# Kernel optimization log

Measured on AMD Instinct MI355X. Metric: run time of the kernel, lower is better.

Reference implementation:

```python
import jax, jax.numpy as jnp
import numpy as np

# Model dims (match init_kwargs)
B_, L, D_MODEL = 1, 2048, 1024
D_INNER, D_CONV, DT_RANK, D_STATE = 2048, 4, 64, 16


def setup_inputs() -> dict:
    key = jax.random.key(0)
    ks = jax.random.split(key, 8)
    s = lambda k, shape, scale: jax.random.normal(k, shape, jnp.float32) * scale
    return {
        "x": jax.random.normal(ks[0], (B_, L, D_MODEL), jnp.float32),
        "in_proj_w": s(ks[1], (D_MODEL, 2 * D_INNER), 0.02),
        "in_proj_b": jnp.zeros((2 * D_INNER,), jnp.float32),
        "conv_w": s(ks[2], (D_CONV, D_INNER), 0.1),          # depthwise kernel, one tap-vector per channel
        "conv_b": jnp.zeros((D_INNER,), jnp.float32),
        "x_proj_w": s(ks[3], (D_INNER, DT_RANK + 2 * D_STATE), 0.02),
        "dt_proj_w": s(ks[4], (DT_RANK, D_INNER), 0.1),
        "dt_proj_b": s(ks[5], (D_INNER,), 0.1),
        "A_log": jnp.log(jnp.tile(jnp.arange(1, D_STATE + 1, dtype=jnp.float32), (D_INNER, 1))),  # S4D-real init
        "D": jnp.ones((D_INNER,), jnp.float32),
        "out_proj_w": s(ks[6], (D_INNER, D_MODEL), 0.02),
        "out_proj_b": jnp.zeros((D_MODEL,), jnp.float32),
    }


def _mamba_forward(x, in_proj_w, in_proj_b, conv_w, conv_b, x_proj_w,
                   dt_proj_w, dt_proj_b, A_log, D, out_proj_w, out_proj_b):
    b, l, _ = x.shape
    d_inner = conv_w.shape[1]
    d_state = A_log.shape[1]

    # in_proj -> split into ssm path and gating residual
    x_and_res = x @ in_proj_w + in_proj_b                 # [b, l, 2*d_inner]
    xin, res = jnp.split(x_and_res, 2, axis=-1)

    # causal depthwise conv1d over the sequence dim (pad left d_conv-1, trunc to l)
    xp = jnp.pad(xin, ((0, 0), (D_CONV - 1, 0), (0, 0)))
    kern = conv_w[:, None, :]                             # [W, I=1, O=d_inner]
    xc = jax.lax.conv_general_dilated(
        xp, kern, window_strides=(1,), padding="VALID",
        dimension_numbers=("NWC", "WIO", "NWC"),
        feature_group_count=d_inner) + conv_b             # [b, l, d_inner]
    u = jax.nn.silu(xc)

    # selective SSM: input-dependent dt, B, C
    A = -jnp.exp(A_log)                                   # [d_inner, d_state]
    dbc = u @ x_proj_w                                    # [b, l, dt_rank + 2*d_state]
    dt, Bm, Cm = jnp.split(dbc, [DT_RANK, DT_RANK + d_state], axis=-1)
    delta = jax.nn.softplus(dt @ dt_proj_w + dt_proj_b)   # [b, l, d_inner]

    deltaA = jnp.exp(jnp.einsum("bld,dn->bldn", delta, A))          # [b, l, d_inner, d_state]
    deltaBu = jnp.einsum("bld,bln,bld->bldn", delta, Bm, u)         # [b, l, d_inner, d_state]

    def step(h, inp):
        dA_t, dBu_t, C_t = inp
        h = dA_t * h + dBu_t                              # [b, d_inner, d_state]
        y_t = jnp.einsum("bdn,bn->bd", h, C_t)
        return h, y_t

    h0 = jnp.zeros((b, d_inner, d_state), u.dtype)
    _, ys = jax.lax.scan(
        step, h0,
        (deltaA.transpose(1, 0, 2, 3), deltaBu.transpose(1, 0, 2, 3), Cm.transpose(1, 0, 2)))
    y = ys.transpose(1, 0, 2) + u * D                     # skip connection via D

    # gate and out-project
    y = y * jax.nn.silu(res)
    return y @ out_proj_w + out_proj_b                    # [b, l, d_model]


def reference(x, in_proj_w, in_proj_b, conv_w, conv_b, x_proj_w,
              dt_proj_w, dt_proj_b, A_log, D, out_proj_w, out_proj_b):
    return _mamba_forward(x, in_proj_w, in_proj_b, conv_w, conv_b, x_proj_w,
                          dt_proj_w, dt_proj_b, A_log, D, out_proj_w, out_proj_b)
```

## Files before the change

### kernel.cpp

```cpp
#include <hip/hip_runtime.h>


#define L_SEQ 2048
#define DMODEL 1024
#define DINNER 2048
#define NSTATE 16
#define DTRANK 64
#define NPROJ_PAD 128
#define NCH 128
#define TCH 16

typedef __attribute__((ext_vector_type(8))) short short8;
typedef __attribute__((ext_vector_type(4))) float f32x4;

__device__ __forceinline__ unsigned short f2bf(float f) {
  unsigned int u = __float_as_uint(f);
  u += 0x7FFFu + ((u >> 16) & 1u);
  return (unsigned short)(u >> 16);
}
__device__ __forceinline__ float bf2f(unsigned short u) {
  return __uint_as_float(((unsigned int)u) << 16);
}

__device__ __forceinline__ void gload16(const void* g, void* l) {
  __builtin_amdgcn_global_load_lds((const __attribute__((address_space(1))) void*)g,
                                   (__attribute__((address_space(3))) void*)l, 16, 0, 0);
}

__global__ void prep_kernel(const float* __restrict__ in_proj_w, const float* __restrict__ x_proj_w,
                            const float* __restrict__ dt_proj_w,
                            const float* __restrict__ out_proj_w, const float* __restrict__ x,
                            unsigned short* __restrict__ w1t, unsigned short* __restrict__ w3t,
                            unsigned short* __restrict__ w4t, unsigned short* __restrict__ w5t,
                            unsigned short* __restrict__ xb) {
  const int bx = blockIdx.x;
  const int tx = threadIdx.x, ty = threadIdx.y;
  const int id = ty * 32 + tx;

  if (bx >= 6464) {
    if (bx < 8512) {
      const int fid = (bx - 6464) * 256 + id;
      f32x4 v = ((const f32x4*)x)[fid];
      ushort4 o;
      o.x = f2bf(v.x); o.y = f2bf(v.y); o.z = f2bf(v.z); o.w = f2bf(v.w);
      ((ushort4*)xb)[fid] = o;
    } else {
      const int fid = (bx - 8512) * 256 + id;
      ((uint4*)(w3t + 96 * 2048))[fid] = (uint4){0, 0, 0, 0};
    }
    return;
  }

  const float* in;
  unsigned short* out;
  int R, C, rel, gx;
  if (bx < 4096) { in = in_proj_w; out = w1t; R = 1024; C = 4096; rel = bx; gx = 128; }
  else if (bx < 4288) { in = x_proj_w; out = w3t; R = 2048; C = 96; rel = bx - 4096; gx = 3; }
  else if (bx < 4416) { in = dt_proj_w; out = w4t; R = 64; C = 2048; rel = bx - 4288; gx = 64; }
  else { in = out_proj_w; out = w5t; R = 2048; C = 1024; rel = bx - 4416; gx = 32; }
  const int c0 = (rel % gx) * 32, r0 = (rel / gx) * 32;

  __shared__ float tile[32][33];
  for (int y = ty; y < 32; y += 8) tile[y][tx] = in[(size_t)(r0 + y) * C + c0 + tx];
  __syncthreads();
  for (int y = ty; y < 32; y += 8) out[(size_t)(c0 + y) * R + r0 + tx] = f2bf(tile[tx][y]);
}

__global__ void conv_silu_kernel(const unsigned short* __restrict__ xin,
                                 const float* __restrict__ cw, const float* __restrict__ cb,
                                 unsigned short* __restrict__ ub) {
  const int id = blockIdx.x * 256 + threadIdx.x;
  const int d = id & (DINNER - 1);
  const int t0 = (id >> 11) * 4;
  float xv[7];
#pragma unroll
  for (int j = 0; j < 7; j++) {
    int tt = t0 - 3 + j;
    xv[j] = (tt >= 0) ? bf2f(xin[(size_t)tt * DINNER + d]) : 0.f;
  }
  float w0 = cw[d], w1 = cw[DINNER + d], w2 = cw[2 * DINNER + d], w3 = cw[3 * DINNER + d];
  const float b = cb[d];
#pragma unroll
  for (int k = 0; k < 4; k++) {
    float acc = b + xv[k] * w0 + xv[k + 1] * w1 + xv[k + 2] * w2 + xv[k + 3] * w3;
    float s = acc / (1.f + __expf(-acc));
    ub[(size_t)(t0 + k) * DINNER + d] = f2bf(s);
  }
}

template <int EPI, int BM, int BN>
__global__ void gemm_bf16(const unsigned short* __restrict__ A,
                          const unsigned short* __restrict__ Bt, float* __restrict__ C,
                          unsigned short* __restrict__ C2, const float* __restrict__ bias, int M,
                          int N, int K, int KS) {
  constexpr int MI = BM / 32, NJ = BN / 32;
  __shared__ __align__(16) unsigned short lA[2][BM * 64];
  __shared__ __align__(16) unsigned short lB[2][BN * 64];
  const int tid = threadIdx.x;
  const int w = tid >> 6;
  const int lane = tid & 63;
  const int m0 = blockIdx.x * BM;
  const int n0 = blockIdx.y * BN;
  const int kbase = blockIdx.z * KS;
  const int lr = lane >> 3;
  const int srcoff = ((lane & 7) ^ lr) * 8;
  const int wm = (w & 1) * (BM / 2);
  const int wn = (w >> 1) * (BN / 2);
  const int ml = lane & 15;
  const int quad = lane >> 4;

  f32x4 acc[MI][NJ];
#pragma unroll
  for (int i = 0; i < MI; i++)
#pragma unroll
    for (int j = 0; j < NJ; j++) acc[i][j] = (f32x4){0.f, 0.f, 0.f, 0.f};

  const unsigned short* Ag = A + (size_t)m0 * K + kbase;
  const unsigned short* Bg = Bt + (size_t)n0 * K + kbase;

  const int niter = KS >> 6;
  auto stage = [&](int buf, int kk) {
#pragma unroll
    for (int c2 = 0; c2 < BM / 32; c2++) {
      const int row = w * (BM / 4) + c2 * 8 + lr;
      gload16(Ag + (size_t)row * K + kk + srcoff, &lA[buf][(w * (BM / 4) + c2 * 8) * 64]);
    }
#pragma unroll
    for (int c2 = 0; c2 < BN / 32; c2++) {
      const int row = w * (BN / 4) + c2 * 8 + lr;
      gload16(Bg + (size_t)row * K + kk + srcoff, &lB[buf][(w * (BN / 4) + c2 * 8) * 64]);
    }
  };

  stage(0, 0);
  for (int it = 0; it < niter; it++) {
    __syncthreads();
    if (it + 1 < niter) stage((it + 1) & 1, (it + 1) << 6);
    const unsigned short* bufA = lA[it & 1];
    const unsigned short* bufB = lB[it & 1];
#pragma unroll
    for (int ks = 0; ks < 2; ks++) {
      short8 af[MI], bfr[NJ];
#pragma unroll
      for (int i = 0; i < MI; i++) {
        const int row = wm + i * 16 + ml;
        af[i] = *(const short8*)&bufA[row * 64 + ((ks * 4 + quad) ^ (ml & 7)) * 8];
      }
#pragma unroll
      for (int j = 0; j < NJ; j++) {
        const int row = wn + j * 16 + ml;
        bfr[j] = *(const short8*)&bufB[row * 64 + ((ks * 4 + quad) ^ (ml & 7)) * 8];
      }
#pragma unroll
      for (int i = 0; i < MI; i++)
#pragma unroll
        for (int j = 0; j < NJ; j++)
          acc[i][j] = __builtin_amdgcn_mfma_f32_16x16x32_bf16(af[i], bfr[j], acc[i][j], 0, 0, 0);
    }
  }

  float* Cp = (EPI == 3) ? C + (size_t)blockIdx.z * M * N : C;
#pragma unroll
  for (int i = 0; i < MI; i++) {
#pragma unroll
    for (int j = 0; j < NJ; j++) {
      const int col = n0 + wn + j * 16 + ml;
      float bv = (EPI == 3) ? 0.f : (bias ? bias[col] : 0.f);
#pragma unroll
      for (int r = 0; r < 4; r++) {
        const int row = m0 + wm + i * 16 + quad * 4 + r;
        float v = acc[i][j][r] + bv;
        if (EPI == 0 || EPI == 3) {
          Cp[(size_t)row * N + col] = v;
        } else if (EPI == 4) {
          if (col < DINNER) {
            ((unsigned short*)C)[(size_t)row * DINNER + col] = f2bf(v);
          } else {
            float s = v / (1.f + __expf(-v));
            C2[(size_t)row * DINNER + (col - DINNER)] = f2bf(s);
          }
        } else if (EPI == 5) {
          float sp = (v > 15.f) ? v : __logf(1.f + __expf(v));
          C2[(size_t)row * N + col] = f2bf(sp);
        }
      }
    }
  }
}

__global__ void reduce_dbc_kernel(const float* __restrict__ part, float* __restrict__ dbc,
                                  unsigned short* __restrict__ dtb) {
  const int id = blockIdx.x * 256 + threadIdx.x;
  float s = 0.f;
#pragma unroll
  for (int z = 0; z < 8; z++) s += part[(size_t)z * (L_SEQ * NPROJ_PAD) + id];
  dbc[id] = s;
  const int col = id & 127;
  if (col < 64) dtb[(id >> 7) * 64 + col] = f2bf(s);
}


__device__ __forceinline__ void load_bc(const float* dbc, int c, float (&Bs)[TCH][NSTATE],
                                        float (&Cs)[TCH][NSTATE], int tid) {
  for (int idx = tid; idx < TCH * 2 * NSTATE; idx += 256) {
    int t = idx >> 5, q = idx & 31;
    float v = dbc[(size_t)(c * TCH + t) * NPROJ_PAD + DTRANK + q];
    if (q < 16) Bs[t][q] = v;
    else Cs[t][q - 16] = v;
  }
}

__global__ void scan1_kernel(const unsigned short* __restrict__ db,
                             const unsigned short* __restrict__ ub, const float* __restrict__ dbc,
                             const float* __restrict__ A_log, unsigned short* __restrict__ P,
                             unsigned short* __restrict__ Hz) {
  __shared__ float Bs[TCH][NSTATE];
  __shared__ float Cs[TCH][NSTATE];
  const int d = blockIdx.x * 256 + threadIdx.x;
  const int c = blockIdx.y;
  load_bc(dbc, c, Bs, Cs, threadIdx.x);
  float Ad[16], h[16], p[16];
#pragma unroll
  for (int n = 0; n < 16; n++) {
    Ad[n] = -__expf(A_log[d * 16 + n]);
    h[n] = 0.f;
    p[n] = 1.f;
  }
  __syncthreads();
#pragma unroll
  for (int t = 0; t < TCH; t++) {
    const int tt = c * TCH + t;
    float dl = bf2f(db[(size_t)tt * DINNER + d]);
    float uu = bf2f(ub[(size_t)tt * DINNER + d]);
    float du = dl * uu;
#pragma unroll
    for (int n = 0; n < 16; n++) {
      float dA = __expf(dl * Ad[n]);
      p[n] *= dA;
      h[n] = dA * h[n] + du * Bs[t][n];
    }
  }
#pragma unroll
  for (int n = 0; n < 16; n++) {
    P[(size_t)(c * 16 + n) * DINNER + d] = f2bf(p[n]);
    Hz[(size_t)(c * 16 + n) * DINNER + d] = f2bf(h[n]);
  }
}

__global__ void scan_carry_kernel(const unsigned short* __restrict__ P,
                                  const unsigned short* __restrict__ Hz,
                                  unsigned short* __restrict__ H0) {
  const int id = blockIdx.x * 256 + threadIdx.x;
  float h = 0.f;
#pragma unroll 8
  for (int c = 0; c < NCH; c++) {
    H0[c * (NSTATE * DINNER) + id] = f2bf(h);
    h = bf2f(P[c * (NSTATE * DINNER) + id]) * h + bf2f(Hz[c * (NSTATE * DINNER) + id]);
  }
}

__global__ void scan2_kernel(const unsigned short* __restrict__ db,
                             const unsigned short* __restrict__ ub, const float* __restrict__ dbc,
                             const float* __restrict__ A_log, const float* __restrict__ Dv,
                             const unsigned short* __restrict__ rsil,
                             const unsigned short* __restrict__ H0,
                             unsigned short* __restrict__ ygb) {
  __shared__ float Bs[TCH][NSTATE];
  __shared__ float Cs[TCH][NSTATE];
  const int d = blockIdx.x * 256 + threadIdx.x;
  const int c = blockIdx.y;
  load_bc(dbc, c, Bs, Cs, threadIdx.x);
  float Ad[16], h[16];
#pragma unroll
  for (int n = 0; n < 16; n++) {
    Ad[n] = -__expf(A_log[d * 16 + n]);
    h[n] = bf2f(H0[(size_t)(c * 16 + n) * DINNER + d]);
  }
  const float Dd = Dv[d];
  __syncthreads();
#pragma unroll
  for (int t = 0; t < TCH; t++) {
    const int tt = c * TCH + t;
    float dl = bf2f(db[(size_t)tt * DINNER + d]);
    float uu = bf2f(ub[(size_t)tt * DINNER + d]);
    float rs = bf2f(rsil[(size_t)tt * DINNER + d]);
    float du = dl * uu;
    float y0 = 0.f, y1 = 0.f;
#pragma unroll
    for (int n = 0; n < 16; n++) {
      float dA = __expf(dl * Ad[n]);
      h[n] = dA * h[n] + du * Bs[t][n];
      if (n & 1) y1 += h[n] * Cs[t][n];
      else y0 += h[n] * Cs[t][n];
    }
    float yg = (y0 + y1 + uu * Dd) * rs;
    ygb[(size_t)tt * DINNER + d] = f2bf(yg);
  }
}


extern "C" void kernel_launch(void* const* d_in, const int* in_sizes, int n_in, void* d_out,
                              int out_size, void* d_ws, size_t ws_size, hipStream_t stream) {
  const float* x = (const float*)d_in[0];
  const float* in_proj_w = (const float*)d_in[1];
  const float* in_proj_b = (const float*)d_in[2];
  const float* conv_w = (const float*)d_in[3];
  const float* conv_b = (const float*)d_in[4];
  const float* x_proj_w = (const float*)d_in[5];
  const float* dt_proj_w = (const float*)d_in[6];
  const float* dt_proj_b = (const float*)d_in[7];
  const float* A_log = (const float*)d_in[8];
  const float* Dvec = (const float*)d_in[9];
  const float* out_proj_w = (const float*)d_in[10];
  const float* out_proj_b = (const float*)d_in[11];
  float* out = (float*)d_out;
  char* ws = (char*)d_ws;
  (void)in_sizes; (void)n_in; (void)out_size; (void)ws_size;

  const size_t MB = 1048576;
  const size_t XB = 0;
  const size_t W1T = 4 * MB;
  const size_t XIN = 12 * MB;
  const size_t RSIL = 20 * MB;
  const size_t UB = 28 * MB;
  const size_t W3T = 36 * MB;
  const size_t DBC = W3T + 524288;
  const size_t DTB = DBC + MB;
  const size_t W4T = DTB + 262144;
  const size_t DELTA = 38 * MB;
  const size_t YGB = 46 * MB;
  const size_t W5T = 54 * MB;
  const size_t G3P = 58 * MB;
  const size_t PB = 66 * MB;
  const size_t HZB = 74 * MB;
  const size_t H0B = 82 * MB;

  prep_kernel<<<8544, dim3(32, 8), 0, stream>>>(
      in_proj_w, x_proj_w, dt_proj_w, out_proj_w, x, (unsigned short*)(ws + W1T),
      (unsigned short*)(ws + W3T), (unsigned short*)(ws + W4T), (unsigned short*)(ws + W5T),
      (unsigned short*)(ws + XB));

  gemm_bf16<4, 128, 128><<<dim3(16, 32, 1), 256, 0, stream>>>(
      (const unsigned short*)(ws + XB), (const unsigned short*)(ws + W1T), (float*)(ws + XIN),
      (unsigned short*)(ws + RSIL), in_proj_b, 2048, 4096, 1024, 1024);

  conv_silu_kernel<<<(L_SEQ * DINNER / 4) / 256, 256, 0, stream>>>(
      (const unsigned short*)(ws + XIN), conv_w, conv_b, (unsigned short*)(ws + UB));

  gemm_bf16<3, 64, 128><<<dim3(32, 1, 8), 256, 0, stream>>>(
      (const unsigned short*)(ws + UB), (const unsigned short*)(ws + W3T), (float*)(ws + G3P),
      nullptr, nullptr, 2048, NPROJ_PAD, 2048, 256);
  reduce_dbc_kernel<<<(L_SEQ * NPROJ_PAD) / 256, 256, 0, stream>>>(
      (const float*)(ws + G3P), (float*)(ws + DBC), (unsigned short*)(ws + DTB));

  gemm_bf16<5, 128, 128><<<dim3(16, 16, 1), 256, 0, stream>>>(
      (const unsigned short*)(ws + DTB), (const unsigned short*)(ws + W4T), nullptr,
      (unsigned short*)(ws + DELTA), dt_proj_b, 2048, 2048, 64, 64);

  {
    const unsigned short* dbp = (const unsigned short*)(ws + DELTA);
    const unsigned short* ubp = (const unsigned short*)(ws + UB);
    const float* dbcp = (const float*)(ws + DBC);
    const unsigned short* rsilp = (const unsigned short*)(ws + RSIL);
    unsigned short* pbp = (unsigned short*)(ws + PB);
    unsigned short* hzp = (unsigned short*)(ws + HZB);
    unsigned short* h0p = (unsigned short*)(ws + H0B);
    unsigned short* ygp = (unsigned short*)(ws + YGB);
    const dim3 sgrid(DINNER / 256, NCH);
    scan1_kernel<<<sgrid, 256, 0, stream>>>(dbp, ubp, dbcp, A_log, pbp, hzp);
    scan_carry_kernel<<<(NSTATE * DINNER) / 256, 256, 0, stream>>>(pbp, hzp, h0p);
    scan2_kernel<<<sgrid, 256, 0, stream>>>(dbp, ubp, dbcp, A_log, Dvec, rsilp, h0p, ygp);
  }

  gemm_bf16<0, 64, 64><<<dim3(32, 16, 1), 256, 0, stream>>>(
      (const unsigned short*)(ws + YGB), (const unsigned short*)(ws + W5T), out, nullptr,
      out_proj_b, 2048, 1024, 2048, 2048);
}
```

Measured before the change: 224.3 us.

## Parallelize carry scan over chunk segments and vectorize conv-silu loads

The chunk-carry kernel, which walked all 128 chunks serially per state element with only 128 blocks, now splits the chunk axis into 8 segments per block. Each segment computes a local affine composition, one warp scans the segment summaries through shared memory, and each segment then replays its chunks to write the carries. This shortens the serial dependency chain and launches eight times as many blocks, at the cost of extra registers and two block barriers. Separately, the conv+silu kernel now handles 8 channels per thread with 16-byte vector loads and stores, cutting per-element memory instructions.

New measurement: 222.7 us. About the same (-0.7%).

```diff
diff --git a/kernel.cpp b/kernel.cpp
--- a/kernel.cpp
+++ b/kernel.cpp
@@ -9,6 +9,8 @@
 #define NPROJ_PAD 128
 #define NCH 128
 #define TCH 16
+#define NSEG 8
+#define SEGLEN 16
 
 typedef __attribute__((ext_vector_type(8))) short short8;
 typedef __attribute__((ext_vector_type(4))) float f32x4;
@@ -70,21 +72,46 @@
                                  const float* __restrict__ cw, const float* __restrict__ cb,
                                  unsigned short* __restrict__ ub) {
   const int id = blockIdx.x * 256 + threadIdx.x;
-  const int d = id & (DINNER - 1);
-  const int t0 = (id >> 11) * 4;
-  float xv[7];
+  const int d0 = (id & 255) * 8;
+  const int t0 = (id >> 8) * 4;
+  float xv[7][8];
 #pragma unroll
   for (int j = 0; j < 7; j++) {
-    int tt = t0 - 3 + j;
-    xv[j] = (tt >= 0) ? bf2f(xin[(size_t)tt * DINNER + d]) : 0.f;
-  }
-  float w0 = cw[d], w1 = cw[DINNER + d], w2 = cw[2 * DINNER + d], w3 = cw[3 * DINNER + d];
-  const float b = cb[d];
+    const int tt = t0 - 3 + j;
+    if (tt >= 0) {
+      short8 v = *(const short8*)&xin[(size_t)tt * DINNER + d0];
+#pragma unroll
+      for (int e = 0; e < 8; e++) xv[j][e] = bf2f((unsigned short)v[e]);
+    } else {
+#pragma unroll
+      for (int e = 0; e < 8; e++) xv[j][e] = 0.f;
+    }
+  }
+  float w[4][8], bb[8];
+#pragma unroll
+  for (int tp = 0; tp < 4; tp++)
+#pragma unroll
+    for (int h = 0; h < 2; h++) {
+      f32x4 a = *(const f32x4*)&cw[tp * DINNER + d0 + h * 4];
+      w[tp][h * 4 + 0] = a.x; w[tp][h * 4 + 1] = a.y;
+      w[tp][h * 4 + 2] = a.z; w[tp][h * 4 + 3] = a.w;
+    }
+#pragma unroll
+  for (int h = 0; h < 2; h++) {
+    f32x4 a = *(const f32x4*)&cb[d0 + h * 4];
+    bb[h * 4 + 0] = a.x; bb[h * 4 + 1] = a.y; bb[h * 4 + 2] = a.z; bb[h * 4 + 3] = a.w;
+  }
 #pragma unroll
   for (int k = 0; k < 4; k++) {
-    float acc = b + xv[k] * w0 + xv[k + 1] * w1 + xv[k + 2] * w2 + xv[k + 3] * w3;
-    float s = acc / (1.f + __expf(-acc));
-    ub[(size_t)(t0 + k) * DINNER + d] = f2bf(s);
+    short8 o;
+#pragma unroll
+    for (int e = 0; e < 8; e++) {
+      float acc = bb[e] + xv[k][e] * w[0][e] + xv[k + 1][e] * w[1][e] + xv[k + 2][e] * w[2][e] +
+                  xv[k + 3][e] * w[3][e];
+      float s = acc / (1.f + __expf(-acc));
+      o[e] = (short)f2bf(s);
+    }
+    *(short8*)&ub[(size_t)(t0 + k) * DINNER + d0] = o;
   }
 }
 
@@ -250,12 +277,41 @@
 __global__ void scan_carry_kernel(const unsigned short* __restrict__ P,
                                   const unsigned short* __restrict__ Hz,
                                   unsigned short* __restrict__ H0) {
-  const int id = blockIdx.x * 256 + threadIdx.x;
-  float h = 0.f;
-#pragma unroll 8
-  for (int c = 0; c < NCH; c++) {
-    H0[c * (NSTATE * DINNER) + id] = f2bf(h);
-    h = bf2f(P[c * (NSTATE * DINNER) + id]) * h + bf2f(Hz[c * (NSTATE * DINNER) + id]);
+  __shared__ float sA[NSEG][32], sB[NSEG][32];
+  const int pl = threadIdx.x & 31;
+  const int sg = threadIdx.x >> 5;
+  const int pair = blockIdx.x * 32 + pl;
+  float pv[SEGLEN], zv[SEGLEN];
+  float A = 1.f, Bc = 0.f;
+#pragma unroll
+  for (int k = 0; k < SEGLEN; k++) {
+    const int c = sg * SEGLEN + k;
+    pv[k] = bf2f(P[(size_t)c * (NSTATE * DINNER) + pair]);
+    zv[k] = bf2f(Hz[(size_t)c * (NSTATE * DINNER) + pair]);
+    A = pv[k] * A;
+    Bc = pv[k] * Bc + zv[k];
+  }
+  sA[sg][pl] = A;
+  sB[sg][pl] = Bc;
+  __syncthreads();
+  if (threadIdx.x < 32) {
+    float a = 1.f, b = 0.f;
+#pragma unroll
+    for (int s = 0; s < NSEG; s++) {
+      float na = sA[s][pl], nb = sB[s][pl];
+      sA[s][pl] = a;
+      sB[s][pl] = b;
+      a = na * a;
+      b = na * b + nb;
+    }
+  }
+  __syncthreads();
+  float h = sB[sg][pl];
+#pragma unroll
+  for (int k = 0; k < SEGLEN; k++) {
+    const int c = sg * SEGLEN + k;
+    H0[(size_t)c * (NSTATE * DINNER) + pair] = f2bf(h);
+    h = pv[k] * h + zv[k];
   }
 }
 
@@ -344,7 +400,7 @@
       (const unsigned short*)(ws + XB), (const unsigned short*)(ws + W1T), (float*)(ws + XIN),
       (unsigned short*)(ws + RSIL), in_proj_b, 2048, 4096, 1024, 1024);
 
-  conv_silu_kernel<<<(L_SEQ * DINNER / 4) / 256, 256, 0, stream>>>(
+  conv_silu_kernel<<<(L_SEQ / 4) * (DINNER / 8) / 256, 256, 0, stream>>>(
       (const unsigned short*)(ws + XIN), conv_w, conv_b, (unsigned short*)(ws + UB));
 
   gemm_bf16<3, 64, 128><<<dim3(32, 1, 8), 256, 0, stream>>>(
@@ -368,7 +424,7 @@
     unsigned short* ygp = (unsigned short*)(ws + YGB);
     const dim3 sgrid(DINNER / 256, NCH);
     scan1_kernel<<<sgrid, 256, 0, stream>>>(dbp, ubp, dbcp, A_log, pbp, hzp);
-    scan_carry_kernel<<<(NSTATE * DINNER) / 256, 256, 0, stream>>>(pbp, hzp, h0p);
+    scan_carry_kernel<<<(NSTATE * DINNER) / 32, 256, 0, stream>>>(pbp, hzp, h0p);
     scan2_kernel<<<sgrid, 256, 0, stream>>>(dbp, ubp, dbcp, A_log, Dvec, rsilp, h0p, ygp);
   }
 
```
